# Performance work log

Measured on AMD Instinct MI355X. Metric: run time of the kernel, lower is better.

The kernel has to match this reference:

```python
import jax, jax.numpy as jnp
import numpy as np

MEAN = jnp.array([0.485, 0.456, 0.406], dtype=jnp.float32).reshape(3, 1, 1)
STD = jnp.array([0.229, 0.224, 0.225], dtype=jnp.float32).reshape(3, 1, 1)
BLOCK = 8  # JPEG DCT block size


def _conv2(x, k):
    # x: [B,H,W], k: [kh,kw] -> SAME conv per image
    kern = k[None, None].astype(x.dtype)
    y = jax.lax.conv_general_dilated(x[:, None], kern, (1, 1), 'SAME')
    return y[:, 0]


def _box3(x):
    return _conv2(x, jnp.ones((3, 3), jnp.float32) / 9.0)


def _normalize(f):
    # per-image min-max to [0,1]; zero map if degenerate (matches _normalize)
    fmin = f.min(axis=(-2, -1), keepdims=True)
    fmax = f.max(axis=(-2, -1), keepdims=True)
    rng = fmax - fmin
    safe = jnp.where(rng < 1e-8, 1.0, rng)
    return jnp.where(rng < 1e-8, 0.0, (f - fmin) / safe)


def _forward(x):
    # denormalize ImageNet stats, clamp, scale to [0,255] (continuous; uint8 round omitted)
    img = jnp.clip(x * STD + MEAN, 0.0, 1.0) * 255.0  # [B,3,H,W]
    gray = 0.299 * img[:, 0] + 0.587 * img[:, 1] + 0.114 * img[:, 2]  # [B,H,W]

    # --- channel 0: spectral residual anomaly (FFT) ---
    F = jnp.fft.fft2(gray)
    logmag = jnp.log(jnp.abs(F) + 1e-8)
    resid = logmag - _box3(logmag)            # high-freq log-spectrum residual
    phase = jnp.angle(F)
    sal = jnp.abs(jnp.fft.ifft2(jnp.exp(resid) * jnp.exp(1j * phase))) ** 2
    M_spec = _normalize(sal)

    # --- channel 1: resampling artifact (2nd-derivative / Laplacian magnitude) ---
    lap_k = jnp.array([[0., 1., 0.], [1., -4., 1.], [0., 1., 0.]], jnp.float32)
    M_resamp = _normalize(jnp.abs(_conv2(gray, lap_k)))

    # --- channel 2: JPEG blockiness (gradient energy on 8x8 block boundaries) ---
    B, H, W = gray.shape
    dh = jnp.abs(gray - jnp.roll(gray, 1, axis=-1))  # horizontal neighbor diff
    dv = jnp.abs(gray - jnp.roll(gray, 1, axis=-2))  # vertical neighbor diff
    col_mask = (jnp.arange(W) % BLOCK == 0).astype(gray.dtype)  # [W]
    row_mask = (jnp.arange(H) % BLOCK == 0).astype(gray.dtype)  # [H]
    blockiness = dh * col_mask[None, None, :] + dv * row_mask[None, :, None]
    M_jpeg = _normalize(blockiness)

    return jnp.stack([M_spec, M_resamp, M_jpeg], axis=1)  # [B,3,H,W]


def setup_inputs() -> dict:
    key = jax.random.key(0)
    x = jax.random.normal(key, (16, 3, 512, 512), dtype=jnp.float32)
    return {"x": x}


def reference(x):
    return _forward(x)
```

## Files before the change

kernel.cpp:

```cpp
#include <hip/hip_runtime.h>
#include <hip/hip_bf16.h>
#include <math.h>

#define W 512
#define H 512
#define HW 262144
#define NB 16

__device__ __forceinline__ int brev9(int x) { return (int)(__brev((unsigned)x) >> 23); }

__device__ __forceinline__ void block_minmax_atomic(float vmin, float vmax,
                                                    unsigned* minU, unsigned* maxU) {
  #pragma unroll
  for (int o = 32; o; o >>= 1) {
    vmin = fminf(vmin, __shfl_xor(vmin, o));
    vmax = fmaxf(vmax, __shfl_xor(vmax, o));
  }
  __shared__ float smin[4], smax[4];
  int wid = threadIdx.x >> 6;
  int lane = threadIdx.x & 63;
  if (lane == 0) { smin[wid] = vmin; smax[wid] = vmax; }
  __syncthreads();
  if (threadIdx.x == 0) {
    float m = smin[0], M = smax[0];
    #pragma unroll
    for (int i = 1; i < 4; ++i) { m = fminf(m, smin[i]); M = fmaxf(M, smax[i]); }
    atomicMin(minU, __float_as_uint(m));
    atomicMax(maxU, __float_as_uint(M));
  }
  __syncthreads();
}

__global__ void k_init(unsigned* mm) {
  int t = threadIdx.x;
  if (t < 48) mm[t] = 0x7F800000u;
  else if (t < 96) mm[t] = 0u;
}

__device__ __forceinline__ float gray_one(float r, float g, float b) {
  float R = fminf(fmaxf(fmaf(r, 0.229f, 0.485f), 0.f), 1.f) * 255.f;
  float G = fminf(fmaxf(fmaf(g, 0.224f, 0.456f), 0.f), 1.f) * 255.f;
  float B = fminf(fmaxf(fmaf(b, 0.225f, 0.406f), 0.f), 1.f) * 255.f;
  return fmaf(0.299f, R, fmaf(0.587f, G, 0.114f * B));
}

__device__ __forceinline__ void tw_init(float2* tw, int t) {
  if (t < 256) {
    float sn, cs;
    __sincosf(-6.283185307179586f * (float)t * (1.f / 512.f), &sn, &cs);
    tw[t] = make_float2(cs, sn);
  }
}

template <int DIR>
__device__ __forceinline__ void fft512_tw(float* sre, float* sim, const float2* tw, int t) {
  #pragma unroll
  for (int s = 1; s <= 9; ++s) {
    __syncthreads();
    int half = 1 << (s - 1);
    int j = t & (half - 1);
    int i0 = ((t >> (s - 1)) << s) + j;
    int i1 = i0 + half;
    float2 w = tw[j << (9 - s)];
    float cs = w.x;
    float sn = (DIR > 0) ? w.y : -w.y;
    float ur = sre[i0], ui = sim[i0];
    float vr = sre[i1], vi = sim[i1];
    float tr = fmaf(vr, cs, -vi * sn);
    float ti = fmaf(vr, sn, vi * cs);
    sre[i0] = ur + tr; sim[i0] = ui + ti;
    sre[i1] = ur - tr; sim[i1] = ui - ti;
  }
  __syncthreads();
}

template <int DIR>
__device__ __forceinline__ void fft512x8_tw(float* sre, float* sim, const float2* tw,
                                            int c, int tc) {
  #pragma unroll
  for (int s = 1; s <= 9; ++s) {
    __syncthreads();
    int half = 1 << (s - 1);
    #pragma unroll
    for (int bb = 0; bb < 8; ++bb) {
      int bf = tc + (bb << 5);
      int j = bf & (half - 1);
      int i0 = ((bf >> (s - 1)) << s) + j;
      int i1 = i0 + half;
      float2 w = tw[j << (9 - s)];
      float cs = w.x;
      float sn = (DIR > 0) ? w.y : -w.y;
      int a0 = i0 * 9 + c, a1 = i1 * 9 + c;
      float ur = sre[a0], ui = sim[a0];
      float vr = sre[a1], vi = sim[a1];
      float tr = fmaf(vr, cs, -vi * sn);
      float ti = fmaf(vr, sn, vi * cs);
      sre[a0] = ur + tr; sim[a0] = ui + ti;
      sre[a1] = ur - tr; sim[a1] = ui - ti;
    }
  }
  __syncthreads();
}

__global__ void k_rowfft(const float* __restrict__ x, float* __restrict__ gray,
                         float2* __restrict__ C) {
  int r = blockIdx.x, b = blockIdx.y, t = threadIdx.x;
  __shared__ float sre[512], sim[512];
  __shared__ float2 tw[256];
  tw_init(tw, t);
  const float* xr = x + (((size_t)(b * 3 + 0)) << 18) + r * W;
  const float* xg = x + (((size_t)(b * 3 + 1)) << 18) + r * W;
  const float* xb = x + (((size_t)(b * 3 + 2)) << 18) + r * W;
  float* gr = gray + (((size_t)b) << 18) + r * W;
  #pragma unroll
  for (int k = t; k < 512; k += 256) {
    float g = gray_one(xr[k], xg[k], xb[k]);
    gr[k] = g;
    int kr = brev9(k);
    sre[kr] = g; sim[kr] = 0.f;
  }
  fft512_tw<1>(sre, sim, tw, t);
  float2* Crow = C + (((size_t)b) << 18) + r * W;
  #pragma unroll
  for (int k = t; k < 512; k += 256) Crow[k] = make_float2(sre[k], sim[k]);
}

__global__ void k_ch12(const float* __restrict__ gray, float* __restrict__ out, unsigned* mm) {
  int slab = blockIdx.x, b = blockIdx.y, t = threadIdx.x;
  const float* gb = gray + (((size_t)b) << 18);
  float* o1 = out + (((size_t)(b * 3 + 1)) << 18);
  float* o2 = out + (((size_t)(b * 3 + 2)) << 18);
  float mn1 = INFINITY, mx1 = -INFINITY, mn2 = INFINITY, mx2 = -INFINITY;
  for (int i4 = t; i4 < 32 * 128; i4 += 256) {
    int r = (slab << 5) + (i4 >> 7);
    int k4 = (i4 & 127) << 2;
    const float* row = gb + r * W;
    float4 c4 = *(const float4*)(row + k4);
    float s_lfw = row[(k4 + W - 1) & (W - 1)];
    float s_rt  = (k4 < W - 4) ? row[k4 + 4] : 0.f;
    float4 up4 = (r > 0)     ? *(const float4*)(gb + (r - 1) * W + k4) : make_float4(0.f, 0.f, 0.f, 0.f);
    float4 dn4 = (r < H - 1) ? *(const float4*)(gb + (r + 1) * W + k4) : make_float4(0.f, 0.f, 0.f, 0.f);
    float c[4]  = {c4.x, c4.y, c4.z, c4.w};
    float up[4] = {up4.x, up4.y, up4.z, up4.w};
    float dn[4] = {dn4.x, dn4.y, dn4.z, dn4.w};
    float lap[4], blk[4];
    #pragma unroll
    for (int e = 0; e < 4; ++e) {
      float lf = (e == 0) ? ((k4 > 0) ? s_lfw : 0.f) : c[e - 1];
      float rt = (e == 3) ? s_rt : c[e + 1];
      lap[e] = fabsf(lf + rt + up[e] + dn[e] - 4.f * c[e]);
      mn1 = fminf(mn1, lap[e]); mx1 = fmaxf(mx1, lap[e]);
    }
    bool rowb = ((r & 7) == 0);
    float pv[4] = {0.f, 0.f, 0.f, 0.f};
    if (rowb) {
      int rp = (r + H - 1) & (H - 1);
      float4 p4 = *(const float4*)(gb + rp * W + k4);
      pv[0] = p4.x; pv[1] = p4.y; pv[2] = p4.z; pv[3] = p4.w;
    }
    #pragma unroll
    for (int e = 0; e < 4; ++e) {
      float v = 0.f;
      if (e == 0 && ((k4 & 7) == 0)) v += fabsf(c[0] - s_lfw);
      if (rowb) v += fabsf(c[e] - pv[e]);
      blk[e] = v;
      mn2 = fminf(mn2, v); mx2 = fmaxf(mx2, v);
    }
    *(float4*)(o1 + r * W + k4) = make_float4(lap[0], lap[1], lap[2], lap[3]);
    *(float4*)(o2 + r * W + k4) = make_float4(blk[0], blk[1], blk[2], blk[3]);
  }
  block_minmax_atomic(mn1, mx1, mm + (b * 3 + 1), mm + 48 + (b * 3 + 1));
  block_minmax_atomic(mn2, mx2, mm + (b * 3 + 2), mm + 48 + (b * 3 + 2));
}

__global__ void k_colfft_fwd(float2* __restrict__ C, float* __restrict__ L) {
  int b = blockIdx.y, col0 = blockIdx.x << 3, t = threadIdx.x;
  __shared__ float sre[512 * 9], sim[512 * 9];
  __shared__ float2 tw[256];
  tw_init(tw, t);
  float2* Cb = C + (((size_t)b) << 18);
  int c = t & 7, q = t >> 3;
  #pragma unroll
  for (int it = 0; it < 16; ++it) {
    int r = (it << 5) + q;
    float2 v = Cb[r * W + col0 + c];
    int rr = brev9(r);
    sre[rr * 9 + c] = v.x; sim[rr * 9 + c] = v.y;
  }
  fft512x8_tw<1>(sre, sim, tw, t >> 5, t & 31);
  float* Lb = L + (((size_t)b) << 18);
  #pragma unroll
  for (int it = 0; it < 16; ++it) {
    int r = (it << 5) + q;
    float re = sre[r * 9 + c], im = sim[r * 9 + c];
    Cb[r * W + col0 + c] = make_float2(re, im);
    Lb[r * W + col0 + c] = logf(sqrtf(fmaf(re, re, im * im)) + 1e-8f);
  }
}

__global__ void k_rowifft_g(float2* __restrict__ C, const float* __restrict__ L) {
  int r = blockIdx.x, b = blockIdx.y, t = threadIdx.x;
  __shared__ float sre[512], sim[512], l0[512], lm[512], lp[512];
  __shared__ float2 tw[256];
  tw_init(tw, t);
  const float* Lb = L + (((size_t)b) << 18);
  #pragma unroll
  for (int k = t; k < 512; k += 256) {
    l0[k] = Lb[r * W + k];
    lm[k] = (r > 0) ? Lb[(r - 1) * W + k] : 0.f;
    lp[k] = (r < H - 1) ? Lb[(r + 1) * W + k] : 0.f;
  }
  __syncthreads();
  float2* Crow = C + (((size_t)b) << 18) + r * W;
  #pragma unroll
  for (int k = t; k < 512; k += 256) {
    float sum = lm[k] + l0[k] + lp[k];
    if (k > 0)     sum += lm[k - 1] + l0[k - 1] + lp[k - 1];
    if (k < W - 1) sum += lm[k + 1] + l0[k + 1] + lp[k + 1];
    float resid = l0[k] - sum * (1.f / 9.f);
    float2 cv = Crow[k];
    float mag = sqrtf(fmaf(cv.x, cv.x, cv.y * cv.y));
    float er = __expf(resid);
    float gr, gi;
    if (mag > 1e-30f) { float tt = er / mag; gr = cv.x * tt; gi = cv.y * tt; }
    else { gr = er; gi = 0.f; }
    int kr = brev9(k);
    sre[kr] = gr; sim[kr] = gi;
  }
  fft512_tw<-1>(sre, sim, tw, t);
  #pragma unroll
  for (int k = t; k < 512; k += 256)
    Crow[k] = make_float2(sre[k] * (1.f / 512.f), sim[k] * (1.f / 512.f));
}

__global__ void k_colifft_sal(const float2* __restrict__ C, float* __restrict__ out, unsigned* mm) {
  int b = blockIdx.y, col0 = blockIdx.x << 3, t = threadIdx.x;
  __shared__ float sre[512 * 9], sim[512 * 9];
  __shared__ float2 tw[256];
  tw_init(tw, t);
  const float2* Cb = C + (((size_t)b) << 18);
  int c = t & 7, q = t >> 3;
  #pragma unroll
  for (int it = 0; it < 16; ++it) {
    int r = (it << 5) + q;
    float2 v = Cb[r * W + col0 + c];
    int rr = brev9(r);
    sre[rr * 9 + c] = v.x; sim[rr * 9 + c] = v.y;
  }
  fft512x8_tw<-1>(sre, sim, tw, t >> 5, t & 31);
  float* ob = out + (((size_t)(b * 3 + 0)) << 18);
  float mn = INFINITY, mx = -INFINITY;
  #pragma unroll
  for (int it = 0; it < 16; ++it) {
    int r = (it << 5) + q;
    float re = sre[r * 9 + c], im = sim[r * 9 + c];
    float sal = fmaf(re, re, im * im) * 3.814697265625e-6f;
    ob[r * W + col0 + c] = sal;
    mn = fminf(mn, sal); mx = fmaxf(mx, sal);
  }
  block_minmax_atomic(mn, mx, mm + b * 3, mm + 48 + b * 3);
}

__global__ void k_norm(float* __restrict__ out, const unsigned* __restrict__ mm) {
  int i = blockIdx.x * blockDim.x + threadIdx.x;
  size_t base = ((size_t)i) << 2;
  int map = (int)(base >> 18);
  float mn = __uint_as_float(mm[map]);
  float mx = __uint_as_float(mm[48 + map]);
  float rng = mx - mn;
  float4 v = *(float4*)(out + base);
  float4 o;
  if (rng < 1e-8f) {
    o = make_float4(0.f, 0.f, 0.f, 0.f);
  } else {
    float inv = 1.f / rng;
    o.x = (v.x - mn) * inv;
    o.y = (v.y - mn) * inv;
    o.z = (v.z - mn) * inv;
    o.w = (v.w - mn) * inv;
  }
  *(float4*)(out + base) = o;
}

extern "C" void kernel_launch(void* const* d_in, const int* in_sizes, int n_in,
                              void* d_out, int out_size, void* d_ws, size_t ws_size,
                              hipStream_t stream) {
  const float* x = (const float*)d_in[0];
  float* out = (float*)d_out;

  float* gray = (float*)d_ws;
  float2* C = (float2*)((char*)d_ws + (size_t)NB * HW * sizeof(float));
  float* L = (float*)((char*)C + (size_t)NB * HW * sizeof(float2));
  unsigned* mm = (unsigned*)((char*)L + (size_t)NB * HW * sizeof(float));

  k_init<<<1, 96, 0, stream>>>(mm);
  k_rowfft<<<dim3(H, NB), 256, 0, stream>>>(x, gray, C);
  k_ch12<<<dim3(16, NB), 256, 0, stream>>>(gray, out, mm);
  k_colfft_fwd<<<dim3(W / 8, NB), 256, 0, stream>>>(C, L);
  k_rowifft_g<<<dim3(H, NB), 256, 0, stream>>>(C, L);
  k_colifft_sal<<<dim3(W / 8, NB), 256, 0, stream>>>(C, out, mm);
  k_norm<<<12288, 256, 0, stream>>>(out, mm);
}
```

Measured before the change: 233.5 us.

## Use radix-4 FFT passes with padded shared memory and half-size row blocks

```diff
diff --git a/kernel.cpp b/kernel.cpp
--- a/kernel.cpp
+++ b/kernel.cpp
@@ -8,6 +8,7 @@
 #define NB 16
 
 __device__ __forceinline__ int brev9(int x) { return (int)(__brev((unsigned)x) >> 23); }
+__device__ __forceinline__ int pad17(int i) { return i + (i >> 4); }
 
 __device__ __forceinline__ void block_minmax_atomic(float vmin, float vmax,
                                                     unsigned* minU, unsigned* maxU) {
@@ -22,9 +23,9 @@
   if (lane == 0) { smin[wid] = vmin; smax[wid] = vmax; }
   __syncthreads();
   if (threadIdx.x == 0) {
+    int nw = (blockDim.x + 63) >> 6;
     float m = smin[0], M = smax[0];
-    #pragma unroll
-    for (int i = 1; i < 4; ++i) { m = fminf(m, smin[i]); M = fmaxf(M, smax[i]); }
+    for (int i = 1; i < nw; ++i) { m = fminf(m, smin[i]); M = fmaxf(M, smax[i]); }
     atomicMin(minU, __float_as_uint(m));
     atomicMax(maxU, __float_as_uint(M));
   }
@@ -44,60 +45,101 @@
   return fmaf(0.299f, R, fmaf(0.587f, G, 0.114f * B));
 }
 
-__device__ __forceinline__ void tw_init(float2* tw, int t) {
-  if (t < 256) {
+__device__ __forceinline__ void tw_init(float2* tw, int t, int nthr) {
+  for (int k = t; k < 256; k += nthr) {
     float sn, cs;
-    __sincosf(-6.283185307179586f * (float)t * (1.f / 512.f), &sn, &cs);
-    tw[t] = make_float2(cs, sn);
-  }
-}
+    __sincosf(-6.283185307179586f * (float)k * (1.f / 512.f), &sn, &cs);
+    tw[k] = make_float2(cs, sn);
+  }
+}
+
+#define QUAD_BODY(LOADA0, LOADA1, LOADA2, LOADA3)                                   \
+  float e0r = sre[LOADA0], e0i = sim[LOADA0];                                       \
+  float e1r = sre[LOADA1], e1i = sim[LOADA1];                                       \
+  float e2r = sre[LOADA2], e2i = sim[LOADA2];                                       \
+  float e3r = sre[LOADA3], e3i = sim[LOADA3];                                       \
+  float t1r = fmaf(e1r, w1c, -e1i * w1s), t1i = fmaf(e1r, w1s, e1i * w1c);          \
+  float t3r = fmaf(e3r, w1c, -e3i * w1s), t3i = fmaf(e3r, w1s, e3i * w1c);          \
+  float A0r = e0r + t1r, A0i = e0i + t1i;                                           \
+  float A1r = e0r - t1r, A1i = e0i - t1i;                                           \
+  float A2r = e2r + t3r, A2i = e2i + t3i;                                           \
+  float A3r = e2r - t3r, A3i = e2i - t3i;                                           \
+  float t2r = fmaf(A2r, w2c, -A2i * w2s), t2i = fmaf(A2r, w2s, A2i * w2c);          \
+  float t4r = fmaf(A3r, w3c, -A3i * w3s), t4i = fmaf(A3r, w3s, A3i * w3c);          \
+  sre[LOADA0] = A0r + t2r; sim[LOADA0] = A0i + t2i;                                 \
+  sre[LOADA2] = A0r - t2r; sim[LOADA2] = A0i - t2i;                                 \
+  sre[LOADA1] = A1r + t4r; sim[LOADA1] = A1i + t4i;                                 \
+  sre[LOADA3] = A1r - t4r; sim[LOADA3] = A1i - t4i;
 
 template <int DIR>
-__device__ __forceinline__ void fft512_tw(float* sre, float* sim, const float2* tw, int t) {
-  #pragma unroll
-  for (int s = 1; s <= 9; ++s) {
+__device__ __forceinline__ void fft512_q(float* sre, float* sim, const float2* tw, int t) {
+  #pragma unroll
+  for (int sp = 1; sp <= 7; sp += 2) {
     __syncthreads();
-    int half = 1 << (s - 1);
-    int j = t & (half - 1);
-    int i0 = ((t >> (s - 1)) << s) + j;
-    int i1 = i0 + half;
-    float2 w = tw[j << (9 - s)];
-    float cs = w.x;
-    float sn = (DIR > 0) ? w.y : -w.y;
-    float ur = sre[i0], ui = sim[i0];
-    float vr = sre[i1], vi = sim[i1];
+    int h = 1 << (sp - 1);
+    int j = t & (h - 1);
+    int q = ((t >> (sp - 1)) << (sp + 1)) + j;
+    float2 w1t = tw[j << (9 - sp)];
+    float2 w2t = tw[j << (8 - sp)];
+    float2 w3t = tw[(j + h) << (8 - sp)];
+    float w1c = w1t.x, w1s = (DIR > 0) ? w1t.y : -w1t.y;
+    float w2c = w2t.x, w2s = (DIR > 0) ? w2t.y : -w2t.y;
+    float w3c = w3t.x, w3s = (DIR > 0) ? w3t.y : -w3t.y;
+    int a0 = pad17(q), a1 = pad17(q + h), a2 = pad17(q + 2 * h), a3 = pad17(q + 3 * h);
+    QUAD_BODY(a0, a1, a2, a3)
+  }
+  __syncthreads();
+  #pragma unroll
+  for (int bb = 0; bb < 2; ++bb) {
+    int bf = t + (bb << 7);
+    float2 w = tw[bf];
+    float cs = w.x, sn = (DIR > 0) ? w.y : -w.y;
+    int a0 = pad17(bf), a1 = pad17(bf + 256);
+    float ur = sre[a0], ui = sim[a0];
+    float vr = sre[a1], vi = sim[a1];
     float tr = fmaf(vr, cs, -vi * sn);
     float ti = fmaf(vr, sn, vi * cs);
-    sre[i0] = ur + tr; sim[i0] = ui + ti;
-    sre[i1] = ur - tr; sim[i1] = ui - ti;
+    sre[a0] = ur + tr; sim[a0] = ui + ti;
+    sre[a1] = ur - tr; sim[a1] = ui - ti;
   }
   __syncthreads();
 }
 
 template <int DIR>
-__device__ __forceinline__ void fft512x8_tw(float* sre, float* sim, const float2* tw,
-                                            int c, int tc) {
-  #pragma unroll
-  for (int s = 1; s <= 9; ++s) {
+__device__ __forceinline__ void fft512x8_q(float* sre, float* sim, const float2* tw,
+                                           int c, int tc) {
+  #pragma unroll
+  for (int sp = 1; sp <= 7; sp += 2) {
     __syncthreads();
-    int half = 1 << (s - 1);
+    int h = 1 << (sp - 1);
     #pragma unroll
-    for (int bb = 0; bb < 8; ++bb) {
-      int bf = tc + (bb << 5);
-      int j = bf & (half - 1);
-      int i0 = ((bf >> (s - 1)) << s) + j;
-      int i1 = i0 + half;
-      float2 w = tw[j << (9 - s)];
-      float cs = w.x;
-      float sn = (DIR > 0) ? w.y : -w.y;
-      int a0 = i0 * 9 + c, a1 = i1 * 9 + c;
-      float ur = sre[a0], ui = sim[a0];
-      float vr = sre[a1], vi = sim[a1];
-      float tr = fmaf(vr, cs, -vi * sn);
-      float ti = fmaf(vr, sn, vi * cs);
-      sre[a0] = ur + tr; sim[a0] = ui + ti;
-      sre[a1] = ur - tr; sim[a1] = ui - ti;
+    for (int m = 0; m < 4; ++m) {
+      int qq = tc + (m << 5);
+      int j = qq & (h - 1);
+      int q = ((qq >> (sp - 1)) << (sp + 1)) + j;
+      float2 w1t = tw[j << (9 - sp)];
+      float2 w2t = tw[j << (8 - sp)];
+      float2 w3t = tw[(j + h) << (8 - sp)];
+      float w1c = w1t.x, w1s = (DIR > 0) ? w1t.y : -w1t.y;
+      float w2c = w2t.x, w2s = (DIR > 0) ? w2t.y : -w2t.y;
+      float w3c = w3t.x, w3s = (DIR > 0) ? w3t.y : -w3t.y;
+      int a0 = q * 9 + c, a1 = (q + h) * 9 + c, a2 = (q + 2 * h) * 9 + c, a3 = (q + 3 * h) * 9 + c;
+      QUAD_BODY(a0, a1, a2, a3)
     }
+  }
+  __syncthreads();
+  #pragma unroll
+  for (int bb = 0; bb < 8; ++bb) {
+    int bf = tc + (bb << 5);
+    float2 w = tw[bf];
+    float cs = w.x, sn = (DIR > 0) ? w.y : -w.y;
+    int a0 = bf * 9 + c, a1 = (bf + 256) * 9 + c;
+    float ur = sre[a0], ui = sim[a0];
+    float vr = sre[a1], vi = sim[a1];
+    float tr = fmaf(vr, cs, -vi * sn);
+    float ti = fmaf(vr, sn, vi * cs);
+    sre[a0] = ur + tr; sim[a0] = ui + ti;
+    sre[a1] = ur - tr; sim[a1] = ui - ti;
   }
   __syncthreads();
 }
@@ -105,24 +147,27 @@
 __global__ void k_rowfft(const float* __restrict__ x, float* __restrict__ gray,
                          float2* __restrict__ C) {
   int r = blockIdx.x, b = blockIdx.y, t = threadIdx.x;
-  __shared__ float sre[512], sim[512];
+  __shared__ float sre[544], sim[544];
   __shared__ float2 tw[256];
-  tw_init(tw, t);
+  tw_init(tw, t, 128);
   const float* xr = x + (((size_t)(b * 3 + 0)) << 18) + r * W;
   const float* xg = x + (((size_t)(b * 3 + 1)) << 18) + r * W;
   const float* xb = x + (((size_t)(b * 3 + 2)) << 18) + r * W;
   float* gr = gray + (((size_t)b) << 18) + r * W;
   #pragma unroll
-  for (int k = t; k < 512; k += 256) {
+  for (int k = t; k < 512; k += 128) {
     float g = gray_one(xr[k], xg[k], xb[k]);
     gr[k] = g;
-    int kr = brev9(k);
+    int kr = pad17(brev9(k));
     sre[kr] = g; sim[kr] = 0.f;
   }
-  fft512_tw<1>(sre, sim, tw, t);
+  fft512_q<1>(sre, sim, tw, t);
   float2* Crow = C + (((size_t)b) << 18) + r * W;
   #pragma unroll
-  for (int k = t; k < 512; k += 256) Crow[k] = make_float2(sre[k], sim[k]);
+  for (int k = t; k < 512; k += 128) {
+    int kp = pad17(k);
+    Crow[k] = make_float2(sre[kp], sim[kp]);
+  }
 }
 
 __global__ void k_ch12(const float* __restrict__ gray, float* __restrict__ out, unsigned* mm) {
@@ -177,7 +222,7 @@
   int b = blockIdx.y, col0 = blockIdx.x << 3, t = threadIdx.x;
   __shared__ float sre[512 * 9], sim[512 * 9];
   __shared__ float2 tw[256];
-  tw_init(tw, t);
+  tw_init(tw, t, 256);
   float2* Cb = C + (((size_t)b) << 18);
   int c = t & 7, q = t >> 3;
   #pragma unroll
@@ -187,7 +232,7 @@
     int rr = brev9(r);
     sre[rr * 9 + c] = v.x; sim[rr * 9 + c] = v.y;
   }
-  fft512x8_tw<1>(sre, sim, tw, t >> 5, t & 31);
+  fft512x8_q<1>(sre, sim, tw, t >> 5, t & 31);
   float* Lb = L + (((size_t)b) << 18);
   #pragma unroll
   for (int it = 0; it < 16; ++it) {
@@ -200,12 +245,12 @@
 
 __global__ void k_rowifft_g(float2* __restrict__ C, const float* __restrict__ L) {
   int r = blockIdx.x, b = blockIdx.y, t = threadIdx.x;
-  __shared__ float sre[512], sim[512], l0[512], lm[512], lp[512];
+  __shared__ float sre[544], sim[544], l0[512], lm[512], lp[512];
   __shared__ float2 tw[256];
-  tw_init(tw, t);
+  tw_init(tw, t, 128);
   const float* Lb = L + (((size_t)b) << 18);
   #pragma unroll
-  for (int k = t; k < 512; k += 256) {
+  for (int k = t; k < 512; k += 128) {
     l0[k] = Lb[r * W + k];
     lm[k] = (r > 0) ? Lb[(r - 1) * W + k] : 0.f;
     lp[k] = (r < H - 1) ? Lb[(r + 1) * W + k] : 0.f;
@@ -213,7 +258,7 @@
   __syncthreads();
   float2* Crow = C + (((size_t)b) << 18) + r * W;
   #pragma unroll
-  for (int k = t; k < 512; k += 256) {
+  for (int k = t; k < 512; k += 128) {
     float sum = lm[k] + l0[k] + lp[k];
     if (k > 0)     sum += lm[k - 1] + l0[k - 1] + lp[k - 1];
     if (k < W - 1) sum += lm[k + 1] + l0[k + 1] + lp[k + 1];
@@ -224,20 +269,22 @@
     float gr, gi;
     if (mag > 1e-30f) { float tt = er / mag; gr = cv.x * tt; gi = cv.y * tt; }
     else { gr = er; gi = 0.f; }
-    int kr = brev9(k);
+    int kr = pad17(brev9(k));
     sre[kr] = gr; sim[kr] = gi;
   }
-  fft512_tw<-1>(sre, sim, tw, t);
-  #pragma unroll
-  for (int k = t; k < 512; k += 256)
-    Crow[k] = make_float2(sre[k] * (1.f / 512.f), sim[k] * (1.f / 512.f));
+  fft512_q<-1>(sre, sim, tw, t);
+  #pragma unroll
+  for (int k = t; k < 512; k += 128) {
+    int kp = pad17(k);
+    Crow[k] = make_float2(sre[kp] * (1.f / 512.f), sim[kp] * (1.f / 512.f));
+  }
 }
 
 __global__ void k_colifft_sal(const float2* __restrict__ C, float* __restrict__ out, unsigned* mm) {
   int b = blockIdx.y, col0 = blockIdx.x << 3, t = threadIdx.x;
   __shared__ float sre[512 * 9], sim[512 * 9];
   __shared__ float2 tw[256];
-  tw_init(tw, t);
+  tw_init(tw, t, 256);
   const float2* Cb = C + (((size_t)b) << 18);
   int c = t & 7, q = t >> 3;
   #pragma unroll
@@ -247,7 +294,7 @@
     int rr = brev9(r);
     sre[rr * 9 + c] = v.x; sim[rr * 9 + c] = v.y;
   }
-  fft512x8_tw<-1>(sre, sim, tw, t >> 5, t & 31);
+  fft512x8_q<-1>(sre, sim, tw, t >> 5, t & 31);
   float* ob = out + (((size_t)(b * 3 + 0)) << 18);
   float mn = INFINITY, mx = -INFINITY;
   #pragma unroll
@@ -294,10 +341,10 @@
   unsigned* mm = (unsigned*)((char*)L + (size_t)NB * HW * sizeof(float));
 
   k_init<<<1, 96, 0, stream>>>(mm);
-  k_rowfft<<<dim3(H, NB), 256, 0, stream>>>(x, gray, C);
+  k_rowfft<<<dim3(H, NB), 128, 0, stream>>>(x, gray, C);
   k_ch12<<<dim3(16, NB), 256, 0, stream>>>(gray, out, mm);
   k_colfft_fwd<<<dim3(W / 8, NB), 256, 0, stream>>>(C, L);
-  k_rowifft_g<<<dim3(H, NB), 256, 0, stream>>>(C, L);
+  k_rowifft_g<<<dim3(H, NB), 128, 0, stream>>>(C, L);
   k_colifft_sal<<<dim3(W / 8, NB), 256, 0, stream>>>(C, out, mm);
   k_norm<<<12288, 256, 0, stream>>>(out, mm);
 }
```

After: 226.7 us. 1.03x faster.
